# Optimization experiments

Hardware: AMD Instinct MI355X
Metric: run time of the kernel (lower is better)

The kernel has to match this reference:

```python
import jax, jax.numpy as jnp
import numpy as np

N = 100000   # nodes (batched graph)
E = 1600000  # edges
G = 2048     # molecules in the batch
D_IN = 128
D_H = 128
MLP_H = 512


def setup_inputs() -> dict:
    key = jax.random.key(0)
    ks = jax.random.split(key, 20)

    def w(k, i, o):
        return (jax.random.normal(k, (i, o), jnp.float32) / np.sqrt(i)).astype(jnp.float32)

    feats = jax.random.normal(ks[0], (N, D_IN), jnp.float32)
    src = jax.random.randint(ks[1], (E,), 0, N)
    dst = jax.random.randint(ks[2], (E,), 0, N)
    graph_ids = jnp.sort(jax.random.randint(ks[3], (N,), 0, G))

    return {
        "feats": feats, "src": src, "dst": dst, "graph_ids": graph_ids,
        # 3 GraphConv layers
        "W0": w(ks[4], D_IN, D_H), "b0": jnp.zeros((D_H,), jnp.float32),
        "W1": w(ks[5], D_H, D_H),  "b1": jnp.zeros((D_H,), jnp.float32),
        "W2": w(ks[6], D_H, D_H),  "b2": jnp.zeros((D_H,), jnp.float32),
        # MLP head: D_H -> 512 -> 256 -> 1
        "Wm0": w(ks[7], D_H, MLP_H),       "bm0": jnp.zeros((MLP_H,), jnp.float32),
        "Wm1": w(ks[8], MLP_H, MLP_H // 2), "bm1": jnp.zeros((MLP_H // 2,), jnp.float32),
        "Wm2": w(ks[9], MLP_H // 2, 1),     "bm2": jnp.zeros((1,), jnp.float32),
    }


def reference(feats, src, dst, graph_ids, W0, b0, W1, b1, W2, b2,
              Wm0, bm0, Wm1, bm1, Wm2, bm2):
    ones_e = jnp.ones((E,), jnp.float32)
    # DGL GraphConv norm='both': D_out^{-1/2} on src, D_in^{-1/2} on dst; deg clamped to 1
    deg_out = jnp.maximum(jax.ops.segment_sum(ones_e, src, num_segments=N), 1.0)
    deg_in = jnp.maximum(jax.ops.segment_sum(ones_e, dst, num_segments=N), 1.0)
    inv_src = jax.lax.rsqrt(deg_out)[:, None]
    inv_dst = jax.lax.rsqrt(deg_in)[:, None]

    def gcn_layer(h, W, b):
        h = h * inv_src                                   # [N, D]
        m = jax.ops.segment_sum(h[src], dst, num_segments=N)  # gather-scatter over edges
        m = m * inv_dst
        return jax.nn.relu(jnp.dot(m, W) + b)

    h = gcn_layer(feats, W0, b0)
    h = gcn_layer(h, W1, b1)
    h = gcn_layer(h, W2, b2)

    # AvgPooling per graph
    counts = jnp.maximum(jax.ops.segment_sum(jnp.ones((N,), jnp.float32), graph_ids, num_segments=G), 1.0)
    emb = jax.ops.segment_sum(h, graph_ids, num_segments=G) / counts[:, None]  # [G, D_H]

    # MLP head (dropout = identity in eval)
    x = jax.nn.relu(jnp.dot(emb, Wm0) + bm0)
    x = jax.nn.relu(jnp.dot(x, Wm1) + bm1)
    return jnp.dot(x, Wm2) + bm2  # [G, 1]
```

## Files before the change

### kernel.cpp

```cpp
#include <hip/hip_runtime.h>


static inline int ceil_div(int a, int b){ return (a + b - 1) / b; }

#define B1 256
#define NBMAX 1024
#define CHUNK_MAX 7168
#define BUCKET_MAX 4096
#define WPREP_BLOCKS 192

typedef __bf16 bf16x8 __attribute__((ext_vector_type(8)));
typedef float  f32x4  __attribute__((ext_vector_type(4)));

static __device__ inline __bf16 bits_to_bf16(unsigned short u){
  union { unsigned short u; __bf16 b; } x; x.u = u; return x.b;
}
static __device__ inline unsigned short bf16_bits(__bf16 b){
  union { __bf16 b; unsigned short u; } x; x.b = b; return x.u;
}
static __device__ inline unsigned pack_split(float s){
  __bf16 h = (__bf16)s;
  __bf16 l = (__bf16)(s - (float)h);
  return ((unsigned)bf16_bits(h) << 16) | (unsigned)bf16_bits(l);
}

__global__ __launch_bounds__(256) void scatter_count_kernel(
    const int* __restrict__ src, const int* __restrict__ dst,
    unsigned* __restrict__ cntA, unsigned* __restrict__ cntB,
    unsigned* __restrict__ stagedA, unsigned char* __restrict__ stagedB,
    const float* __restrict__ W0, const float* __restrict__ W1,
    const float* __restrict__ W2, __bf16* __restrict__ Wsp,
    int E, int NB){
  if (blockIdx.x >= B1){
    int gidx = (blockIdx.x - B1)*256 + threadIdx.x;
    if (gidx < 3*128*128){
      int layer = gidx >> 14, idx = gidx & 16383;
      const float* W = layer == 0 ? W0 : (layer == 1 ? W1 : W2);
      int k = idx >> 7, n = idx & 127;
      float w = W[idx];
      __bf16 h = (__bf16)w;
      __bf16 l = (__bf16)(w - (float)h);
      Wsp[(size_t)layer*2*16384 + n*128 + k] = h;
      Wsp[(size_t)layer*2*16384 + 16384 + n*128 + k] = l;
    }
    return;
  }

  __shared__ unsigned la[NBMAX], lb[NBMAX];
  __shared__ unsigned tsum[256];
  __shared__ unsigned stA[CHUNK_MAX];
  __shared__ unsigned char stB[CHUNK_MAX];

  const int t = threadIdx.x;
  const int blk = blockIdx.x;
  const int chunk = (E + B1 - 1) / B1;
  const int e0 = blk * chunk, e1 = min(e0 + chunk, E);
  const int len = e1 - e0;
  const int strideB = (chunk + 3) & ~3;

  #pragma unroll
  for (int i = t; i < NBMAX; i += 256){ la[i] = 0u; lb[i] = 0u; }
  __syncthreads();
  for (int e = e0 + t; e < e1; e += 256){
    atomicAdd(&la[dst[e] >> 7], 1u);
    atomicAdd(&lb[src[e] >> 7], 1u);
  }
  __syncthreads();

  for (int job = 0; job < 2; job++){
    unsigned* lx = job ? lb : la;
    unsigned* cx = job ? cntB : cntA;
    int b4 = t*4;
    unsigned v0 = lx[b4], v1 = lx[b4+1], v2 = lx[b4+2], v3 = lx[b4+3];
    unsigned s = v0+v1+v2+v3;
    tsum[t] = s;
    __syncthreads();
    for (int off = 1; off < 256; off <<= 1){
      unsigned u = (t >= off) ? tsum[t-off] : 0u;
      __syncthreads();
      tsum[t] += u;
      __syncthreads();
    }
    unsigned run = tsum[t] - s;
    unsigned o0 = run, o1 = run+v0, o2 = run+v0+v1, o3 = run+v0+v1+v2;
    lx[b4] = o0; lx[b4+1] = o1; lx[b4+2] = o2; lx[b4+3] = o3;
    if (b4   < NB) cx[(size_t)blk*NB + b4  ] = o0;
    if (b4+1 < NB) cx[(size_t)blk*NB + b4+1] = o1;
    if (b4+2 < NB) cx[(size_t)blk*NB + b4+2] = o2;
    if (b4+3 < NB) cx[(size_t)blk*NB + b4+3] = o3;
    __syncthreads();
  }

  for (int e = e0 + t; e < e1; e += 256){
    int s = src[e], d = dst[e];
    unsigned pA = atomicAdd(&la[d >> 7], 1u);
    stA[pA] = ((unsigned)(d & 127) << 17) | (unsigned)s;
    unsigned pB = atomicAdd(&lb[s >> 7], 1u);
    stB[pB] = (unsigned char)(s & 127);
  }
  __syncthreads();

  for (int i = t; i < len; i += 256)
    stagedA[(size_t)blk*chunk + i] = stA[i];
  int w4 = (len + 3) >> 2;
  unsigned* gB = (unsigned*)(stagedB + (size_t)blk*strideB);
  for (int i = t; i < w4; i += 256)
    gB[i] = *(unsigned*)&stB[4*i];
}

__global__ void totals_kernel(const unsigned* __restrict__ cntA,
                              const unsigned* __restrict__ cntB,
                              unsigned* __restrict__ totals, int NB, int E){
  int b = blockIdx.x * 256 + threadIdx.x;
  if (b >= NB) return;
  const unsigned* cx = blockIdx.y ? cntB : cntA;
  const int chunk = (E + B1 - 1) / B1;
  unsigned run = 0;
  for (int blk = 0; blk < B1; blk++){
    int lenb = E - blk*chunk; if (lenb > chunk) lenb = chunk; if (lenb < 0) lenb = 0;
    unsigned cur = cx[(size_t)blk*NB + b];
    unsigned nxt = (b < NB-1) ? cx[(size_t)blk*NB + b + 1] : (unsigned)lenb;
    run += nxt - cur;
  }
  totals[(size_t)blockIdx.y*NB + b] = run;
}

__global__ void scan_base_kernel(const unsigned* __restrict__ totals,
                                 unsigned* __restrict__ baseA, unsigned* __restrict__ baseB,
                                 int NB, int E){
  __shared__ unsigned s[NBMAX];
  int t = threadIdx.x;
  for (int job = 0; job < 2; job++){
    unsigned* base = job ? baseB : baseA;
    unsigned x = (t < NB) ? totals[(size_t)job*NB + t] : 0u;
    s[t] = x;
    __syncthreads();
    for (int off = 1; off < NBMAX; off <<= 1){
      unsigned v = (t >= off) ? s[t - off] : 0u;
      __syncthreads();
      s[t] += v;
      __syncthreads();
    }
    if (t < NB) base[t] = s[t] - x;
    if (t == 0) base[NB] = (unsigned)E;
    __syncthreads();
  }
}

__global__ __launch_bounds__(256) void csr_finalize_kernel(
    const unsigned* __restrict__ stagedA, const unsigned char* __restrict__ stagedB,
    const unsigned* __restrict__ cntA, const unsigned* __restrict__ cntB,
    const unsigned* __restrict__ baseA,
    int* __restrict__ row_ptr, float* __restrict__ inv_dst, float* __restrict__ inv_src,
    int* __restrict__ col, int N, int E, int NB){
  __shared__ unsigned offs[256];
  __shared__ unsigned segbase[257];
  __shared__ unsigned tsum[256];
  __shared__ unsigned edge[BUCKET_MAX];
  __shared__ unsigned sorted[BUCKET_MAX];
  __shared__ unsigned cnt[128];
  __shared__ unsigned scn[128];

  const int b = blockIdx.x, t = threadIdx.x;
  const int node0 = b << 7;
  const int nn = min(128, N - node0);
  const int chunk = (E + B1 - 1) / B1;
  const int strideB = (chunk + 3) & ~3;
  int lenb_t = E - t*chunk; if (lenb_t > chunk) lenb_t = chunk; if (lenb_t < 0) lenb_t = 0;

  {
    unsigned o0 = cntA[(size_t)t*NB + b];
    unsigned o1 = (b < NB-1) ? cntA[(size_t)t*NB + b + 1] : (unsigned)lenb_t;
    unsigned len = o1 - o0;
    offs[t] = o0;
    tsum[t] = len;
    __syncthreads();
    for (int off = 1; off < 256; off <<= 1){
      unsigned u = (t >= off) ? tsum[t-off] : 0u;
      __syncthreads();
      tsum[t] += u;
      __syncthreads();
    }
    segbase[t] = tsum[t] - len;
    if (t == 255) segbase[256] = tsum[255];
    __syncthreads();
    int bucketlen = (int)segbase[256];

    for (int idx = t; idx < bucketlen; idx += 256){
      int lo = 0, hi = 255;
      while (lo < hi){ int m = (lo + hi + 1) >> 1; if (segbase[m] <= (unsigned)idx) lo = m; else hi = m - 1; }
      edge[idx] = stagedA[(size_t)lo*chunk + offs[lo] + ((unsigned)idx - segbase[lo])];
    }
    if (t < 128) cnt[t] = 0u;
    __syncthreads();
    for (int idx = t; idx < bucketlen; idx += 256)
      atomicAdd(&cnt[(edge[idx] >> 17) & 127u], 1u);
    __syncthreads();
    unsigned mycnt = (t < 128) ? cnt[t] : 0u;
    if (t < 128) scn[t] = mycnt;
    __syncthreads();
    for (int off = 1; off < 128; off <<= 1){
      unsigned v = (t < 128 && t >= off) ? scn[t - off] : 0u;
      __syncthreads();
      if (t < 128) scn[t] += v;
      __syncthreads();
    }
    int e0 = (int)baseA[b];
    if (t < nn){
      unsigned excl = scn[t] - mycnt;
      row_ptr[node0 + t] = e0 + (int)excl;
      unsigned c = mycnt < 1u ? 1u : mycnt;
      inv_dst[node0 + t] = rsqrtf((float)c);
      cnt[t] = excl;
    }
    if (b == NB - 1 && t == 0) row_ptr[N] = E;
    __syncthreads();
    for (int idx = t; idx < bucketlen; idx += 256){
      unsigned v = edge[idx];
      unsigned p = atomicAdd(&cnt[(v >> 17) & 127u], 1u);
      sorted[p] = v & 0x1FFFFu;
    }
    __syncthreads();
    for (int idx = t; idx < bucketlen; idx += 256)
      col[e0 + idx] = (int)sorted[idx];
  }

  __syncthreads();
  {
    unsigned o0 = cntB[(size_t)t*NB + b];
    unsigned o1 = (b < NB-1) ? cntB[(size_t)t*NB + b + 1] : (unsigned)lenb_t;
    unsigned len = o1 - o0;
    offs[t] = o0;
    tsum[t] = len;
    __syncthreads();
    for (int off = 1; off < 256; off <<= 1){
      unsigned u = (t >= off) ? tsum[t-off] : 0u;
      __syncthreads();
      tsum[t] += u;
      __syncthreads();
    }
    segbase[t] = tsum[t] - len;
    if (t == 255) segbase[256] = tsum[255];
    if (t < 128) cnt[t] = 0u;
    __syncthreads();
    int bucketlen = (int)segbase[256];
    unsigned char* edgeB = (unsigned char*)edge;
    for (int idx = t; idx < bucketlen; idx += 256){
      int lo = 0, hi = 255;
      while (lo < hi){ int m = (lo + hi + 1) >> 1; if (segbase[m] <= (unsigned)idx) lo = m; else hi = m - 1; }
      edgeB[idx] = stagedB[(size_t)lo*strideB + offs[lo] + ((unsigned)idx - segbase[lo])];
    }
    __syncthreads();
    for (int idx = t; idx < bucketlen; idx += 256)
      atomicAdd(&cnt[edgeB[idx]], 1u);
    __syncthreads();
    if (t < nn){
      unsigned c = cnt[t] < 1u ? 1u : cnt[t];
      inv_src[node0 + t] = rsqrtf((float)c);
    }
  }
}

template<bool SC>
__global__ __launch_bounds__(256) void csr_agg_kernel(
    const int* __restrict__ row_ptr, const int* __restrict__ col,
    const float* __restrict__ hs, const float* __restrict__ scale,
    const float* __restrict__ inv_dst, unsigned* __restrict__ aggp, int N){
  int node = (int)((blockIdx.x*256u + threadIdx.x) >> 5);
  int lane = threadIdx.x & 31;
  if (node >= N) return;
  int r0 = row_ptr[node];
  int r1 = row_ptr[node+1];
  float4 a0 = make_float4(0.f,0.f,0.f,0.f);
  float4 a1 = make_float4(0.f,0.f,0.f,0.f);
  float4 a2 = make_float4(0.f,0.f,0.f,0.f);
  float4 a3 = make_float4(0.f,0.f,0.f,0.f);
  int e = r0;
  for (; e + 3 < r1; e += 4){
    int s0 = col[e], s1 = col[e+1], s2 = col[e+2], s3 = col[e+3];
    float4 v0 = ((const float4*)(hs + (size_t)s0*128))[lane];
    float4 v1 = ((const float4*)(hs + (size_t)s1*128))[lane];
    float4 v2 = ((const float4*)(hs + (size_t)s2*128))[lane];
    float4 v3 = ((const float4*)(hs + (size_t)s3*128))[lane];
    if (SC){
      float c0 = scale[s0], c1 = scale[s1], c2 = scale[s2], c3 = scale[s3];
      v0.x*=c0; v0.y*=c0; v0.z*=c0; v0.w*=c0;
      v1.x*=c1; v1.y*=c1; v1.z*=c1; v1.w*=c1;
      v2.x*=c2; v2.y*=c2; v2.z*=c2; v2.w*=c2;
      v3.x*=c3; v3.y*=c3; v3.z*=c3; v3.w*=c3;
    }
    a0.x += v0.x; a0.y += v0.y; a0.z += v0.z; a0.w += v0.w;
    a1.x += v1.x; a1.y += v1.y; a1.z += v1.z; a1.w += v1.w;
    a2.x += v2.x; a2.y += v2.y; a2.z += v2.z; a2.w += v2.w;
    a3.x += v3.x; a3.y += v3.y; a3.z += v3.z; a3.w += v3.w;
  }
  for (; e < r1; e++){
    int s0 = col[e];
    float4 v0 = ((const float4*)(hs + (size_t)s0*128))[lane];
    if (SC){ float c0 = scale[s0]; v0.x*=c0; v0.y*=c0; v0.z*=c0; v0.w*=c0; }
    a0.x += v0.x; a0.y += v0.y; a0.z += v0.z; a0.w += v0.w;
  }
  float idst = inv_dst[node];
  float rx = ((a0.x + a1.x) + (a2.x + a3.x)) * idst;
  float ry = ((a0.y + a1.y) + (a2.y + a3.y)) * idst;
  float rz = ((a0.z + a1.z) + (a2.z + a3.z)) * idst;
  float rw = ((a0.w + a1.w) + (a2.w + a3.w)) * idst;
  uint4 p;
  p.x = pack_split(rx); p.y = pack_split(ry);
  p.z = pack_split(rz); p.w = pack_split(rw);
  ((uint4*)(aggp + (size_t)node*128))[lane] = p;
}

__global__ __launch_bounds__(256) void mfma_gemm_kernel(
    const unsigned* __restrict__ A,
    const __bf16* __restrict__ Whi, const __bf16* __restrict__ Wlo,
    const float* __restrict__ bias, const float* __restrict__ out_scale,
    float* __restrict__ out, int M){
  __shared__ __bf16 BhL[128*40];
  __shared__ __bf16 BlL[128*40];

  const int tid  = threadIdx.x;
  const int wv   = tid >> 6;
  const int lane = tid & 63;
  const int q    = lane >> 4;
  const int mn   = lane & 15;
  const int row0 = blockIdx.x*128 + wv*32;

  f32x4 acc[2][8];
  #pragma unroll
  for (int mt = 0; mt < 2; mt++)
    #pragma unroll
    for (int nt = 0; nt < 8; nt++)
      acc[mt][nt] = (f32x4){0.f,0.f,0.f,0.f};

  #pragma unroll
  for (int kc = 0; kc < 4; kc++){
    __syncthreads();
    for (int i = tid; i < 128*4; i += 256){
      int n = i >> 2, c = (i & 3) << 3;
      *(bf16x8*)&BhL[n*40 + c] = *(const bf16x8*)(Whi + n*128 + kc*32 + c);
      *(bf16x8*)&BlL[n*40 + c] = *(const bf16x8*)(Wlo + n*128 + kc*32 + c);
    }
    __syncthreads();

    bf16x8 ah[2], al[2];
    #pragma unroll
    for (int mt = 0; mt < 2; mt++){
      const unsigned* ap = A + (size_t)(row0 + mt*16 + mn)*128 + kc*32 + q*8;
      uint4 x0 = *(const uint4*)ap;
      uint4 x1 = *(const uint4*)(ap + 4);
      unsigned v[8] = {x0.x, x0.y, x0.z, x0.w, x1.x, x1.y, x1.z, x1.w};
      #pragma unroll
      for (int j = 0; j < 8; j++){
        ah[mt][j] = bits_to_bf16((unsigned short)(v[j] >> 16));
        al[mt][j] = bits_to_bf16((unsigned short)(v[j] & 0xFFFFu));
      }
    }
    #pragma unroll
    for (int nt = 0; nt < 8; nt++){
      int boff = (nt*16 + mn)*40 + q*8;
      bf16x8 bh = *(const bf16x8*)&BhL[boff];
      bf16x8 bl = *(const bf16x8*)&BlL[boff];
      #pragma unroll
      for (int mt = 0; mt < 2; mt++){
        acc[mt][nt] = __builtin_amdgcn_mfma_f32_16x16x32_bf16(al[mt], bh, acc[mt][nt], 0, 0, 0);
        acc[mt][nt] = __builtin_amdgcn_mfma_f32_16x16x32_bf16(ah[mt], bl, acc[mt][nt], 0, 0, 0);
        acc[mt][nt] = __builtin_amdgcn_mfma_f32_16x16x32_bf16(ah[mt], bh, acc[mt][nt], 0, 0, 0);
      }
    }
  }

  #pragma unroll
  for (int mt = 0; mt < 2; mt++){
    #pragma unroll
    for (int r = 0; r < 4; r++){
      int gm = row0 + mt*16 + q*4 + r;
      if (gm < M){
        float osc = out_scale ? out_scale[gm] : 1.f;
        #pragma unroll
        for (int nt = 0; nt < 8; nt++){
          float v = acc[mt][nt][r] + bias[nt*16 + mn];
          v = fmaxf(v, 0.f) * osc;
          out[(size_t)gm*128 + nt*16 + mn] = v;
        }
      }
    }
  }
}

__global__ __launch_bounds__(256) void head_kernel(
    const float* __restrict__ h, const int* __restrict__ gid,
    const float* __restrict__ Wm0, const float* __restrict__ bm0,
    const float* __restrict__ Wm1, const float* __restrict__ bm1,
    const float* __restrict__ Wm2, const float* __restrict__ bm2,
    float* __restrict__ out, int N, int G){
  __shared__ float embL[8][128];
  __shared__ float x1L[8][512];
  __shared__ float x2L[8][256];

  const int t = threadIdx.x;
  const int wave = t >> 6, lane = t & 63;
  const int g0 = blockIdx.x * 8;

  for (int gg = 0; gg < 2; gg++){
    int gl = wave*2 + gg;
    int g = g0 + gl;
    float ax = 0.f, ay = 0.f;
    int start = 0, end = 0;
    if (g < G){
      int lo = 0, hi = N;
      while (lo < hi){ int mid = (lo + hi) >> 1; if (gid[mid] < g) lo = mid + 1; else hi = mid; }
      start = lo;
      hi = N;
      while (lo < hi){ int mid = (lo + hi) >> 1; if (gid[mid] <= g) lo = mid + 1; else hi = mid; }
      end = lo;
      for (int n = start; n < end; n++){
        float2 v = ((const float2*)(h + (size_t)n*128))[lane];
        ax += v.x; ay += v.y;
      }
    }
    int c = end - start; if (c < 1) c = 1;
    float invc = 1.0f / (float)c;
    embL[gl][2*lane]   = ax * invc;
    embL[gl][2*lane+1] = ay * invc;
  }
  __syncthreads();

  {
    float acc[8][2];
    #pragma unroll
    for (int g = 0; g < 8; g++){ acc[g][0] = 0.f; acc[g][1] = 0.f; }
    for (int k = 0; k < 128; k++){
      float w0 = Wm0[(size_t)k*512 + t];
      float w1 = Wm0[(size_t)k*512 + t + 256];
      #pragma unroll
      for (int g = 0; g < 8; g++){
        float e = embL[g][k];
        acc[g][0] = fmaf(e, w0, acc[g][0]);
        acc[g][1] = fmaf(e, w1, acc[g][1]);
      }
    }
    float b0v = bm0[t], b1v = bm0[t + 256];
    #pragma unroll
    for (int g = 0; g < 8; g++){
      x1L[g][t]       = fmaxf(acc[g][0] + b0v, 0.f);
      x1L[g][t + 256] = fmaxf(acc[g][1] + b1v, 0.f);
    }
  }
  __syncthreads();

  {
    float acc[8];
    #pragma unroll
    for (int g = 0; g < 8; g++) acc[g] = 0.f;
    for (int k = 0; k < 512; k++){
      float w = Wm1[(size_t)k*256 + t];
      #pragma unroll
      for (int g = 0; g < 8; g++)
        acc[g] = fmaf(x1L[g][k], w, acc[g]);
    }
    float bv = bm1[t];
    #pragma unroll
    for (int g = 0; g < 8; g++)
      x2L[g][t] = fmaxf(acc[g] + bv, 0.f);
  }
  __syncthreads();

  {
    int g = t >> 5;
    int c = t & 31;
    float s = 0.f;
    for (int i = c; i < 256; i += 32)
      s = fmaf(x2L[g][i], Wm2[i], s);
    for (int off = 16; off > 0; off >>= 1) s += __shfl_down(s, off, 32);
    if (c == 0 && (g0 + g) < G) out[g0 + g] = s + bm2[0];
  }
}

extern "C" void kernel_launch(void* const* d_in, const int* in_sizes, int n_in,
                              void* d_out, int out_size, void* d_ws, size_t ws_size,
                              hipStream_t stream){
  const float* feats = (const float*)d_in[0];
  const int*   src   = (const int*)d_in[1];
  const int*   dst   = (const int*)d_in[2];
  const int*   gid   = (const int*)d_in[3];
  const float* W0 = (const float*)d_in[4];   const float* b0 = (const float*)d_in[5];
  const float* W1 = (const float*)d_in[6];   const float* b1 = (const float*)d_in[7];
  const float* W2 = (const float*)d_in[8];   const float* b2 = (const float*)d_in[9];
  const float* Wm0 = (const float*)d_in[10]; const float* bm0 = (const float*)d_in[11];
  const float* Wm1 = (const float*)d_in[12]; const float* bm1 = (const float*)d_in[13];
  const float* Wm2 = (const float*)d_in[14]; const float* bm2 = (const float*)d_in[15];
  float* out = (float*)d_out;

  const int E   = in_sizes[1];
  const int N   = in_sizes[3];
  const int G   = out_size;
  const int NB  = ceil_div(N, 128);
  const int chunk = ceil_div(E, B1);
  const int strideB = (chunk + 3) & ~3;

  char* ws = (char*)d_ws;
  size_t off = 0;
  auto carve = [&](size_t bytes) -> char* {
    off = (off + 255) & ~(size_t)255;
    char* p = ws + off; off += bytes; return p;
  };
  float* inv_src = (float*)carve((size_t)N*4);
  float* inv_dst = (float*)carve((size_t)N*4);
  int* row_ptr = (int*)carve((size_t)(N+1)*4);
  int* col     = (int*)carve((size_t)E*4);
  __bf16* Wsp = (__bf16*)carve(6*128*128*2);
  float* hs  = (float*)carve((size_t)N*128*4);
  unsigned* aggp = (unsigned*)carve((size_t)N*128*4);

  unsigned* T = (unsigned*)aggp;
  unsigned* cntA   = T;
  unsigned* cntB   = cntA + (size_t)B1*NB;
  unsigned* totals = cntB + (size_t)B1*NB;
  unsigned* baseA  = totals + 2*(size_t)NB;
  unsigned* baseB  = baseA + (NB+1);
  unsigned* stagedA = baseB + (NB+1);
  unsigned char* stagedB = (unsigned char*)(stagedA + (size_t)B1*chunk);

  scatter_count_kernel<<<B1 + WPREP_BLOCKS, 256, 0, stream>>>(
      src, dst, cntA, cntB, stagedA, stagedB, W0, W1, W2, Wsp, E, NB);
  totals_kernel<<<dim3(ceil_div(NB,256), 2), 256, 0, stream>>>(cntA, cntB, totals, NB, E);
  scan_base_kernel<<<1, NBMAX, 0, stream>>>(totals, baseA, baseB, NB, E);
  csr_finalize_kernel<<<NB, 256, 0, stream>>>(stagedA, stagedB, cntA, cntB, baseA,
                                              row_ptr, inv_dst, inv_src, col, N, E, NB);

  const int agg_blocks = ceil_div(N*32, 256);
  const int ggrid = ceil_div(N, 128);
  __bf16 *Whi0 = Wsp,            *Wlo0 = Wsp + 16384;
  __bf16 *Whi1 = Wsp + 2*16384,  *Wlo1 = Wsp + 3*16384;
  __bf16 *Whi2 = Wsp + 4*16384,  *Wlo2 = Wsp + 5*16384;
  csr_agg_kernel<true><<<agg_blocks, 256, 0, stream>>>(row_ptr, col, feats, inv_src, inv_dst, aggp, N);
  mfma_gemm_kernel<<<ggrid, 256, 0, stream>>>(aggp, Whi0, Wlo0, b0, inv_src, hs, N);
  csr_agg_kernel<false><<<agg_blocks, 256, 0, stream>>>(row_ptr, col, hs, nullptr, inv_dst, aggp, N);
  mfma_gemm_kernel<<<ggrid, 256, 0, stream>>>(aggp, Whi1, Wlo1, b1, inv_src, hs, N);
  csr_agg_kernel<false><<<agg_blocks, 256, 0, stream>>>(row_ptr, col, hs, nullptr, inv_dst, aggp, N);
  mfma_gemm_kernel<<<ggrid, 256, 0, stream>>>(aggp, Whi2, Wlo2, b2, nullptr, hs, N);
  head_kernel<<<ceil_div(G,8), 256, 0, stream>>>(hs, gid, Wm0, bm0, Wm1, bm1, Wm2, bm2, out, N, G);
}
```

Measured before the change: 699.9 us.

## Fuse CSR aggregation with MFMA GEMM per 32-row tile via LDS

Each layer now runs one kernel instead of two. A single 64-thread wave gathers and aggregates 32 destination nodes into LDS as split bf16 pairs, then multiplies that tile against the weights with MFMA directly. This removes the write and re-read of the N x 128 intermediate aggregate buffer and two launches per layer. Weights are now read straight from global memory with no LDS staging, and outputs ping-pong between two buffers. In exchange, each block holds a single wave that handles 16 nodes in sequence. That lowers the number of gather loads in flight per CU and can leave the latency-bound gather underutilized.

```diff
diff --git a/kernel.cpp b/kernel.cpp
--- a/kernel.cpp
+++ b/kernel.cpp
@@ -262,69 +262,67 @@
 }
 
 template<bool SC>
-__global__ __launch_bounds__(256) void csr_agg_kernel(
+__global__ __launch_bounds__(64) void fused_agg_gemm_kernel(
     const int* __restrict__ row_ptr, const int* __restrict__ col,
-    const float* __restrict__ hs, const float* __restrict__ scale,
-    const float* __restrict__ inv_dst, unsigned* __restrict__ aggp, int N){
-  int node = (int)((blockIdx.x*256u + threadIdx.x) >> 5);
-  int lane = threadIdx.x & 31;
-  if (node >= N) return;
-  int r0 = row_ptr[node];
-  int r1 = row_ptr[node+1];
-  float4 a0 = make_float4(0.f,0.f,0.f,0.f);
-  float4 a1 = make_float4(0.f,0.f,0.f,0.f);
-  float4 a2 = make_float4(0.f,0.f,0.f,0.f);
-  float4 a3 = make_float4(0.f,0.f,0.f,0.f);
-  int e = r0;
-  for (; e + 3 < r1; e += 4){
-    int s0 = col[e], s1 = col[e+1], s2 = col[e+2], s3 = col[e+3];
-    float4 v0 = ((const float4*)(hs + (size_t)s0*128))[lane];
-    float4 v1 = ((const float4*)(hs + (size_t)s1*128))[lane];
-    float4 v2 = ((const float4*)(hs + (size_t)s2*128))[lane];
-    float4 v3 = ((const float4*)(hs + (size_t)s3*128))[lane];
-    if (SC){
-      float c0 = scale[s0], c1 = scale[s1], c2 = scale[s2], c3 = scale[s3];
-      v0.x*=c0; v0.y*=c0; v0.z*=c0; v0.w*=c0;
-      v1.x*=c1; v1.y*=c1; v1.z*=c1; v1.w*=c1;
-      v2.x*=c2; v2.y*=c2; v2.z*=c2; v2.w*=c2;
-      v3.x*=c3; v3.y*=c3; v3.z*=c3; v3.w*=c3;
-    }
-    a0.x += v0.x; a0.y += v0.y; a0.z += v0.z; a0.w += v0.w;
-    a1.x += v1.x; a1.y += v1.y; a1.z += v1.z; a1.w += v1.w;
-    a2.x += v2.x; a2.y += v2.y; a2.z += v2.z; a2.w += v2.w;
-    a3.x += v3.x; a3.y += v3.y; a3.z += v3.z; a3.w += v3.w;
-  }
-  for (; e < r1; e++){
-    int s0 = col[e];
-    float4 v0 = ((const float4*)(hs + (size_t)s0*128))[lane];
-    if (SC){ float c0 = scale[s0]; v0.x*=c0; v0.y*=c0; v0.z*=c0; v0.w*=c0; }
-    a0.x += v0.x; a0.y += v0.y; a0.z += v0.z; a0.w += v0.w;
-  }
-  float idst = inv_dst[node];
-  float rx = ((a0.x + a1.x) + (a2.x + a3.x)) * idst;
-  float ry = ((a0.y + a1.y) + (a2.y + a3.y)) * idst;
-  float rz = ((a0.z + a1.z) + (a2.z + a3.z)) * idst;
-  float rw = ((a0.w + a1.w) + (a2.w + a3.w)) * idst;
-  uint4 p;
-  p.x = pack_split(rx); p.y = pack_split(ry);
-  p.z = pack_split(rz); p.w = pack_split(rw);
-  ((uint4*)(aggp + (size_t)node*128))[lane] = p;
-}
-
-__global__ __launch_bounds__(256) void mfma_gemm_kernel(
-    const unsigned* __restrict__ A,
+    const float* __restrict__ hs_in, const float* __restrict__ scale,
+    const float* __restrict__ inv_dst,
     const __bf16* __restrict__ Whi, const __bf16* __restrict__ Wlo,
     const float* __restrict__ bias, const float* __restrict__ out_scale,
-    float* __restrict__ out, int M){
-  __shared__ __bf16 BhL[128*40];
-  __shared__ __bf16 BlL[128*40];
-
-  const int tid  = threadIdx.x;
-  const int wv   = tid >> 6;
-  const int lane = tid & 63;
-  const int q    = lane >> 4;
-  const int mn   = lane & 15;
-  const int row0 = blockIdx.x*128 + wv*32;
+    float* __restrict__ out, int N){
+  __shared__ unsigned Apk[32*132];
+
+  const int lane = threadIdx.x;
+  const int half = lane >> 5;
+  const int l32  = lane & 31;
+  const int row0 = blockIdx.x * 32;
+
+  for (int i = 0; i < 16; i++){
+    int j = i*2 + half;
+    int node = row0 + j;
+    float4 a0 = make_float4(0.f,0.f,0.f,0.f);
+    float4 a1 = make_float4(0.f,0.f,0.f,0.f);
+    float4 a2 = make_float4(0.f,0.f,0.f,0.f);
+    float4 a3 = make_float4(0.f,0.f,0.f,0.f);
+    int e = 0, r1 = 0;
+    if (node < N){ e = row_ptr[node]; r1 = row_ptr[node+1]; }
+    for (; e + 3 < r1; e += 4){
+      int s0 = col[e], s1 = col[e+1], s2 = col[e+2], s3 = col[e+3];
+      float4 v0 = ((const float4*)(hs_in + (size_t)s0*128))[l32];
+      float4 v1 = ((const float4*)(hs_in + (size_t)s1*128))[l32];
+      float4 v2 = ((const float4*)(hs_in + (size_t)s2*128))[l32];
+      float4 v3 = ((const float4*)(hs_in + (size_t)s3*128))[l32];
+      if (SC){
+        float c0 = scale[s0], c1 = scale[s1], c2 = scale[s2], c3 = scale[s3];
+        v0.x*=c0; v0.y*=c0; v0.z*=c0; v0.w*=c0;
+        v1.x*=c1; v1.y*=c1; v1.z*=c1; v1.w*=c1;
+        v2.x*=c2; v2.y*=c2; v2.z*=c2; v2.w*=c2;
+        v3.x*=c3; v3.y*=c3; v3.z*=c3; v3.w*=c3;
+      }
+      a0.x += v0.x; a0.y += v0.y; a0.z += v0.z; a0.w += v0.w;
+      a1.x += v1.x; a1.y += v1.y; a1.z += v1.z; a1.w += v1.w;
+      a2.x += v2.x; a2.y += v2.y; a2.z += v2.z; a2.w += v2.w;
+      a3.x += v3.x; a3.y += v3.y; a3.z += v3.z; a3.w += v3.w;
+    }
+    for (; e < r1; e++){
+      int s0 = col[e];
+      float4 v0 = ((const float4*)(hs_in + (size_t)s0*128))[l32];
+      if (SC){ float c0 = scale[s0]; v0.x*=c0; v0.y*=c0; v0.z*=c0; v0.w*=c0; }
+      a0.x += v0.x; a0.y += v0.y; a0.z += v0.z; a0.w += v0.w;
+    }
+    float idst = (node < N) ? inv_dst[node] : 0.f;
+    float rx = ((a0.x + a1.x) + (a2.x + a3.x)) * idst;
+    float ry = ((a0.y + a1.y) + (a2.y + a3.y)) * idst;
+    float rz = ((a0.z + a1.z) + (a2.z + a3.z)) * idst;
+    float rw = ((a0.w + a1.w) + (a2.w + a3.w)) * idst;
+    uint4 p;
+    p.x = pack_split(rx); p.y = pack_split(ry);
+    p.z = pack_split(rz); p.w = pack_split(rw);
+    *(uint4*)&Apk[j*132 + l32*4] = p;
+  }
+  __syncthreads();
+
+  const int q  = lane >> 4;
+  const int mn = lane & 15;
 
   f32x4 acc[2][8];
   #pragma unroll
@@ -335,32 +333,25 @@
 
   #pragma unroll
   for (int kc = 0; kc < 4; kc++){
-    __syncthreads();
-    for (int i = tid; i < 128*4; i += 256){
-      int n = i >> 2, c = (i & 3) << 3;
-      *(bf16x8*)&BhL[n*40 + c] = *(const bf16x8*)(Whi + n*128 + kc*32 + c);
-      *(bf16x8*)&BlL[n*40 + c] = *(const bf16x8*)(Wlo + n*128 + kc*32 + c);
-    }
-    __syncthreads();
-
     bf16x8 ah[2], al[2];
     #pragma unroll
     for (int mt = 0; mt < 2; mt++){
-      const unsigned* ap = A + (size_t)(row0 + mt*16 + mn)*128 + kc*32 + q*8;
+      const unsigned* ap = &Apk[(mt*16 + mn)*132 + kc*32 + q*8];
       uint4 x0 = *(const uint4*)ap;
       uint4 x1 = *(const uint4*)(ap + 4);
       unsigned v[8] = {x0.x, x0.y, x0.z, x0.w, x1.x, x1.y, x1.z, x1.w};
       #pragma unroll
-      for (int j = 0; j < 8; j++){
-        ah[mt][j] = bits_to_bf16((unsigned short)(v[j] >> 16));
-        al[mt][j] = bits_to_bf16((unsigned short)(v[j] & 0xFFFFu));
+      for (int jj = 0; jj < 8; jj++){
+        ah[mt][jj] = bits_to_bf16((unsigned short)(v[jj] >> 16));
+        al[mt][jj] = bits_to_bf16((unsigned short)(v[jj] & 0xFFFFu));
       }
     }
     #pragma unroll
     for (int nt = 0; nt < 8; nt++){
-      int boff = (nt*16 + mn)*40 + q*8;
-      bf16x8 bh = *(const bf16x8*)&BhL[boff];
-      bf16x8 bl = *(const bf16x8*)&BlL[boff];
+      const __bf16* bhp = Whi + (nt*16 + mn)*128 + kc*32 + q*8;
+      const __bf16* blp = Wlo + (nt*16 + mn)*128 + kc*32 + q*8;
+      bf16x8 bh = *(const bf16x8*)bhp;
+      bf16x8 bl = *(const bf16x8*)blp;
       #pragma unroll
       for (int mt = 0; mt < 2; mt++){
         acc[mt][nt] = __builtin_amdgcn_mfma_f32_16x16x32_bf16(al[mt], bh, acc[mt][nt], 0, 0, 0);
@@ -375,7 +366,7 @@
     #pragma unroll
     for (int r = 0; r < 4; r++){
       int gm = row0 + mt*16 + q*4 + r;
-      if (gm < M){
+      if (gm < N){
         float osc = out_scale ? out_scale[gm] : 1.f;
         #pragma unroll
         for (int nt = 0; nt < 8; nt++){
@@ -510,10 +501,10 @@
   int* row_ptr = (int*)carve((size_t)(N+1)*4);
   int* col     = (int*)carve((size_t)E*4);
   __bf16* Wsp = (__bf16*)carve(6*128*128*2);
-  float* hs  = (float*)carve((size_t)N*128*4);
-  unsigned* aggp = (unsigned*)carve((size_t)N*128*4);
-
-  unsigned* T = (unsigned*)aggp;
+  float* hsA = (float*)carve((size_t)N*128*4);
+  float* hsB = (float*)carve((size_t)N*128*4);
+
+  unsigned* T = (unsigned*)hsB;
   unsigned* cntA   = T;
   unsigned* cntB   = cntA + (size_t)B1*NB;
   unsigned* totals = cntB + (size_t)B1*NB;
@@ -529,16 +520,15 @@
   csr_finalize_kernel<<<NB, 256, 0, stream>>>(stagedA, stagedB, cntA, cntB, baseA,
                                               row_ptr, inv_dst, inv_src, col, N, E, NB);
 
-  const int agg_blocks = ceil_div(N*32, 256);
-  const int ggrid = ceil_div(N, 128);
+  const int fgrid = ceil_div(N, 32);
   __bf16 *Whi0 = Wsp,            *Wlo0 = Wsp + 16384;
   __bf16 *Whi1 = Wsp + 2*16384,  *Wlo1 = Wsp + 3*16384;
   __bf16 *Whi2 = Wsp + 4*16384,  *Wlo2 = Wsp + 5*16384;
-  csr_agg_kernel<true><<<agg_blocks, 256, 0, stream>>>(row_ptr, col, feats, inv_src, inv_dst, aggp, N);
-  mfma_gemm_kernel<<<ggrid, 256, 0, stream>>>(aggp, Whi0, Wlo0, b0, inv_src, hs, N);
-  csr_agg_kernel<false><<<agg_blocks, 256, 0, stream>>>(row_ptr, col, hs, nullptr, inv_dst, aggp, N);
-  mfma_gemm_kernel<<<ggrid, 256, 0, stream>>>(aggp, Whi1, Wlo1, b1, inv_src, hs, N);
-  csr_agg_kernel<false><<<agg_blocks, 256, 0, stream>>>(row_ptr, col, hs, nullptr, inv_dst, aggp, N);
-  mfma_gemm_kernel<<<ggrid, 256, 0, stream>>>(aggp, Whi2, Wlo2, b2, nullptr, hs, N);
-  head_kernel<<<ceil_div(G,8), 256, 0, stream>>>(hs, gid, Wm0, bm0, Wm1, bm1, Wm2, bm2, out, N, G);
-}
+  fused_agg_gemm_kernel<true><<<fgrid, 64, 0, stream>>>(
+      row_ptr, col, feats, inv_src, inv_dst, Whi0, Wlo0, b0, inv_src, hsA, N);
+  fused_agg_gemm_kernel<false><<<fgrid, 64, 0, stream>>>(
+      row_ptr, col, hsA, nullptr, inv_dst, Whi1, Wlo1, b1, inv_src, hsB, N);
+  fused_agg_gemm_kernel<false><<<fgrid, 64, 0, stream>>>(
+      row_ptr, col, hsB, nullptr, inv_dst, Whi2, Wlo2, b2, nullptr, hsA, N);
+  head_kernel<<<ceil_div(G,8), 256, 0, stream>>>(hsA, gid, Wm0, bm0, Wm1, bm1, Wm2, bm2, out, N, G);
+}
```

New measurement: 907.5 us. 29.7% more time.
